# Kernel optimization log

Measured on AMD Instinct MI355X. Metric: run time of the kernel, lower is better.

The kernel has to match this reference:

```python
import jax, jax.numpy as jnp
import numpy as np

CHEB_K = 2  # hops per support; stacked terms = 1 + 2*CHEB_K = 5


def setup_inputs() -> dict:
    key = jax.random.key(0)
    k1, k2, k3, k4, k5 = jax.random.split(key, 5)
    B, N, C, O, D = 16, 1024, 64, 64, 10
    return {
        "x": jax.random.normal(k1, (B, N, C), dtype=jnp.float32),
        "adj": jax.random.uniform(k2, (2, B, N, N), dtype=jnp.float32),
        "node_embedding": jax.random.normal(k3, (N, D), dtype=jnp.float32),
        "weights_pool": jax.random.normal(k4, (D, 2 * CHEB_K + 1, C, O), dtype=jnp.float32) * 0.1,
        "bias_pool": jax.random.normal(k5, (D, O), dtype=jnp.float32) * 0.1,
    }


def reference(x, adj, node_embedding, weights_pool, bias_pool):
    # k-hop graph aggregation over each of the 2 supports
    out = [x]
    for s in range(adj.shape[0]):
        a = adj[s]  # [B, N, N]
        x1 = x
        for _ in range(CHEB_K):
            x1 = jnp.einsum('bnm,bmc->bnc', a, x1)
            out.append(x1)
    x_g = jnp.stack(out, axis=2)  # [B, N, K, C] with K = 2*cheb_k+1 (already node-major)
    # per-node hypernetwork weights and bias from node embeddings
    weights = jnp.einsum('nd,dkio->nkio', node_embedding, weights_pool)  # [N, K, C, O]
    bias = node_embedding @ bias_pool  # [N, O]
    # per-node contraction over (K, C)
    return jnp.einsum('bnki,nkio->bno', x_g, weights) + bias
```

## Files before the change

### kernel.cpp

```cpp
#include <hip/hip_runtime.h>
#include <stdint.h>


typedef __attribute__((ext_vector_type(4))) float f32x4;
typedef __attribute__((ext_vector_type(2))) float f32x2;
typedef __attribute__((ext_vector_type(8))) short s16x8;
typedef __attribute__((ext_vector_type(8))) __bf16 bf16x8;

__device__ __forceinline__ unsigned short f2bf(float f) {
  union { float f; uint32_t u; } v; v.f = f;
  uint32_t r = v.u + 0x7FFFu + ((v.u >> 16) & 1u);
  return (unsigned short)(r >> 16);
}
__device__ __forceinline__ uint32_t pack2(float a, float b) {
  return (uint32_t)f2bf(a) | ((uint32_t)f2bf(b) << 16);
}

union FragU { s16x8 s; bf16x8 b; uint32_t u[4]; };

__device__ __forceinline__ void async_cp16(const void* g, void* l) {
  __builtin_amdgcn_global_load_lds(
      (const __attribute__((address_space(1))) void*)g,
      (__attribute__((address_space(3))) void*)l, 16, 0, 0);
}

__global__ __launch_bounds__(256) void cvtprep(
    const float* __restrict__ adj, unsigned short* __restrict__ adjb,
    const float* __restrict__ x, const float* __restrict__ wp,
    unsigned short* __restrict__ XT0, unsigned short* __restrict__ X0b,
    unsigned short* __restrict__ wpTb) {
  __shared__ __align__(16) char smem[17160];
  const int tid = threadIdx.x;
  const int bid = blockIdx.x;

  if (bid < 8192) {
    const size_t stride = (size_t)8192 * 256 * 8;
    for (size_t p = ((size_t)bid * 256 + tid) * 8; p < 33554432u;
         p += stride) {
      f32x4 a = *(const f32x4*)(adj + p);
      f32x4 b = *(const f32x4*)(adj + p + 4);
      union { s16x8 s; uint32_t u[4]; } o;
      o.u[0] = pack2(a[0], a[1]);
      o.u[1] = pack2(a[2], a[3]);
      o.u[2] = pack2(b[0], b[1]);
      o.u[3] = pack2(b[2], b[3]);
      *(s16x8*)(adjb + p) = o.s;
    }
    return;
  }

  const int pid = bid - 8192;
  if (pid < 256) {
    unsigned short (*tl)[72] = (unsigned short(*)[72])smem;
    const int b = pid >> 4, n0 = (pid & 15) * 64;
    {
      const int c4 = (tid & 15) * 4;
#pragma unroll
      for (int i = 0; i < 4; ++i) {
        const int row = (tid >> 4) + i * 16;
        f32x4 v =
            *(const f32x4*)(x + ((size_t)(b * 1024 + n0 + row)) * 64 + c4);
        const uint32_t w0 = pack2(v[0], v[1]);
        const uint32_t w1 = pack2(v[2], v[3]);
        *(uint32_t*)&tl[row][c4]     = w0;
        *(uint32_t*)&tl[row][c4 + 2] = w1;
        const uint64_t wq = (uint64_t)w0 | ((uint64_t)w1 << 32);
        *(uint64_t*)(X0b + ((size_t)(b * 1024 + n0 + row)) * 64 + c4) = wq;
      }
    }
    __syncthreads();
    {
      const int c = tid >> 2;
      const int nch = (tid & 3) * 16;
      s16x8 s0, s1;
#pragma unroll
      for (int j = 0; j < 8; ++j) {
        s0[j] = (short)tl[nch + j][c];
        s1[j] = (short)tl[nch + 8 + j][c];
      }
      unsigned short* p = XT0 + (size_t)(b * 64 + c) * 1024 + n0 + nch;
      *(s16x8*)p = s0;
      *(s16x8*)(p + 8) = s1;
    }
  } else {
    float (*tl)[65] = (float(*)[65])smem;
    const int jj = pid - 256;
    const int d = jj / 5, ki0 = (jj % 5) * 64;
    const float* src = wp + (size_t)d * 20480;
    {
      const int o4 = (tid & 15) * 4;
#pragma unroll
      for (int i = 0; i < 4; ++i) {
        const int row = (tid >> 4) + i * 16;
        f32x4 v = *(const f32x4*)(src + (size_t)(ki0 + row) * 64 + o4);
        tl[row][o4] = v[0]; tl[row][o4 + 1] = v[1];
        tl[row][o4 + 2] = v[2]; tl[row][o4 + 3] = v[3];
      }
    }
    __syncthreads();
    {
      const int o = tid >> 2;
      const int kch = (tid & 3) * 16;
      unsigned short* dst =
          wpTb + (size_t)d * 20480 + (size_t)o * 320 + ki0 + kch;
      s16x8 s0, s1;
#pragma unroll
      for (int j = 0; j < 8; ++j) {
        s0[j] = (short)f2bf(tl[kch + j][o]);
        s1[j] = (short)f2bf(tl[kch + 8 + j][o]);
      }
      *(s16x8*)dst = s0;
      *(s16x8*)(dst + 8) = s1;
    }
  }
}

__device__ __forceinline__ void hop_body(
    char* smem, const unsigned short* __restrict__ A,
    const unsigned short* __restrict__ XT, unsigned short* __restrict__ Xoutb,
    unsigned short* __restrict__ XTout, int write_xt, int rowbase) {
  const int tid = threadIdx.x;
  const int wave = tid >> 6, lane = tid & 63;
  const int l15 = lane & 15, q = lane >> 4;

  unsigned short* const Ast = (unsigned short*)smem;
  unsigned short* const Bst = (unsigned short*)smem + 12288;

  const int sub = lane >> 3;
  const int ch = lane & 7;
  const unsigned short* asrc[2];
  const unsigned short* bsrc[2];
  int ldso[2];
#pragma unroll
  for (int i = 0; i < 2; ++i) {
    const int r = wave * 16 + i * 8 + sub;
    asrc[i] = A + (size_t)(rowbase + r) * 1024 + (ch ^ (r & 7)) * 8;
    bsrc[i] = XT + (size_t)r * 1024 + (ch ^ (r & 7)) * 8;
    ldso[i] = (wave * 16 + i * 8) * 64;
  }

  f32x4 acc[4];
#pragma unroll
  for (int t = 0; t < 4; ++t) acc[t] = (f32x4){0.f, 0.f, 0.f, 0.f};

  auto issue = [&](int s, int k0) {
#pragma unroll
    for (int i = 0; i < 2; ++i) {
      async_cp16(asrc[i] + k0, Ast + s * 4096 + ldso[i]);
      async_cp16(bsrc[i] + k0, Bst + s * 4096 + ldso[i]);
    }
  };
  const int sw = l15 & 7;
  auto compute = [&](int s) {
    const unsigned short* Ab = Ast + s * 4096 + (wave * 16 + l15) * 64;
    const unsigned short* Bb = Bst + s * 4096 + l15 * 64;
#pragma unroll
    for (int h = 0; h < 2; ++h) {
      const int cko = ((h * 4 + q) ^ sw) * 8;
      FragU af;
      af.s = *(const s16x8*)(Ab + cko);
#pragma unroll
      for (int t = 0; t < 4; ++t) {
        FragU bf;
        bf.s = *(const s16x8*)(Bb + t * 1024 + cko);
        acc[t] = __builtin_amdgcn_mfma_f32_16x16x32_bf16(af.b, bf.b, acc[t],
                                                         0, 0, 0);
      }
    }
  };

  issue(0, 0);
  issue(1, 64);
#pragma unroll 1
  for (int kt = 0; kt < 15; ++kt) {
    asm volatile("s_waitcnt vmcnt(4)" ::: "memory");
    __builtin_amdgcn_sched_barrier(0);
    __builtin_amdgcn_s_barrier();
    __builtin_amdgcn_sched_barrier(0);
    if (kt < 14) issue((kt + 2) % 3, (kt + 2) * 64);
    compute(kt % 3);
  }
  asm volatile("s_waitcnt vmcnt(0)" ::: "memory");
  __builtin_amdgcn_sched_barrier(0);
  __builtin_amdgcn_s_barrier();
  __builtin_amdgcn_sched_barrier(0);
  compute(0);

  __syncthreads();
  float (*tile)[65] = (float(*)[65])smem;
#pragma unroll
  for (int t = 0; t < 4; ++t)
#pragma unroll
    for (int rr = 0; rr < 4; ++rr)
      tile[wave * 16 + q * 4 + rr][t * 16 + l15] = acc[t][rr];
  __syncthreads();

  {
    const int row = tid >> 2;
    const int cb = (tid & 3) * 16;
    unsigned short* __restrict__ outp =
        Xoutb + (size_t)(rowbase + row) * 64 + cb;
    s16x8 s0, s1;
#pragma unroll
    for (int j = 0; j < 8; ++j) {
      s0[j] = (short)f2bf(tile[row][cb + j]);
      s1[j] = (short)f2bf(tile[row][cb + 8 + j]);
    }
    *(s16x8*)outp = s0;
    *(s16x8*)(outp + 8) = s1;
  }
  if (write_xt) {
    const int c = tid >> 2;
    const int nch = (tid & 3) * 16;
    unsigned short* __restrict__ xtp = XTout + (size_t)c * 1024 + rowbase + nch;
    s16x8 s0, s1;
#pragma unroll
    for (int j = 0; j < 8; ++j) {
      s0[j] = (short)f2bf(tile[nch + j][c]);
      s1[j] = (short)f2bf(tile[nch + 8 + j][c]);
    }
    *(s16x8*)xtp = s0;
    *(s16x8*)(xtp + 8) = s1;
  }
}

__global__ __launch_bounds__(256, 2) void hop1_kernel(
    const unsigned short* __restrict__ adjb,
    const unsigned short* __restrict__ XT0, unsigned short* __restrict__ X1b,
    unsigned short* __restrict__ XT1) {
  __shared__ __align__(16) char smem[49152];
  const int bx = blockIdx.x, slice = blockIdx.y, b = slice & 15;
  hop_body(smem, adjb + (size_t)slice * 1048576, XT0 + (size_t)b * 65536,
           X1b + (size_t)slice * 65536, XT1 + (size_t)slice * 65536, 1,
           bx * 64);
}

__global__ __launch_bounds__(256, 2) void hop2_kernel(
    const unsigned short* __restrict__ adjb,
    const unsigned short* __restrict__ XT1, unsigned short* __restrict__ X2b) {
  __shared__ __align__(16) char smem[49152];
  const int bx = 15 - (int)blockIdx.x;
  const int slice = 31 - (int)blockIdx.y;
  hop_body(smem, adjb + (size_t)slice * 1048576, XT1 + (size_t)slice * 65536,
           X2b + (size_t)slice * 65536, (unsigned short*)0, 0, bx * 64);
}

__global__ __launch_bounds__(256, 2) void final_kernel(
    const unsigned short* __restrict__ X0b,
    const unsigned short* __restrict__ X1b,
    const unsigned short* __restrict__ X2b,
    const unsigned short* __restrict__ wpTb, const float* __restrict__ emb,
    const float* __restrict__ bias_pool, float* __restrict__ out) {
  __shared__ unsigned short xg[2][16][328];
  const int tid = threadIdx.x;
  const int node_base = blockIdx.x * 2;

  for (int u = tid; u < 5120; u += 256) {
    const int nd = u / 2560;
    int rem = u - nd * 2560;
    const int bb = rem / 160;
    const int kiu = rem - bb * 160;
    const int ki = kiu * 2;
    const int k = ki >> 6;
    const int c = ki & 63;
    const int nn = node_base + nd;
    const unsigned short* base =
        k == 0 ? X0b
        : k == 1 ? X1b
        : k == 2 ? X2b
        : k == 3 ? X1b + 1048576 : X2b + 1048576;
    const uint32_t w =
        *(const uint32_t*)(base + ((size_t)bb * 1024 + nn) * 64 + c);
    *(uint32_t*)&xg[nd][bb][ki] = w;
  }
  __syncthreads();

  const int wave = tid >> 6, lane = tid & 63;
  const int nd = wave >> 1, oh = wave & 1;
  const int l15 = lane & 15, q = lane >> 4;
  const int n = node_base + nd;

  FragU af[10];
#pragma unroll
  for (int ks = 0; ks < 10; ++ks)
    af[ks].s = *(const s16x8*)&xg[nd][l15][ks * 32 + q * 8];

  f32x4 acc[2];
  acc[0] = (f32x4){0.f, 0.f, 0.f, 0.f};
  acc[1] = (f32x4){0.f, 0.f, 0.f, 0.f};

  const unsigned short* wb0 = wpTb + (size_t)(oh * 32 + l15) * 320 + q * 8;
#pragma unroll 1
  for (int d = 0; d < 10; ++d) {
    const unsigned short* wd = wb0 + (size_t)d * 20480;
    f32x4 tmp[2];
    tmp[0] = (f32x4){0.f, 0.f, 0.f, 0.f};
    tmp[1] = (f32x4){0.f, 0.f, 0.f, 0.f};
#pragma unroll
    for (int ks = 0; ks < 10; ++ks) {
#pragma unroll
      for (int tt = 0; tt < 2; ++tt) {
        FragU bf;
        bf.s = *(const s16x8*)(wd + tt * 5120 + ks * 32);
        tmp[tt] = __builtin_amdgcn_mfma_f32_16x16x32_bf16(af[ks].b, bf.b,
                                                          tmp[tt], 0, 0, 0);
      }
    }
    const float e = emb[n * 10 + d];
#pragma unroll
    for (int tt = 0; tt < 2; ++tt)
#pragma unroll
      for (int rr = 0; rr < 4; ++rr)
        acc[tt][rr] += e * tmp[tt][rr];
  }

#pragma unroll
  for (int tt = 0; tt < 2; ++tt) {
    const int o = (oh * 2 + tt) * 16 + l15;
    float bv = 0.f;
#pragma unroll
    for (int d = 0; d < 10; ++d)
      bv += emb[n * 10 + d] * bias_pool[d * 64 + o];
#pragma unroll
    for (int rr = 0; rr < 4; ++rr) {
      const int bb = q * 4 + rr;
      out[((size_t)bb * 1024 + n) * 64 + o] = acc[tt][rr] + bv;
    }
  }
}

extern "C" void kernel_launch(void* const* d_in, const int* in_sizes, int n_in,
                              void* d_out, int out_size, void* d_ws,
                              size_t ws_size, hipStream_t stream) {
  const float* x   = (const float*)d_in[0];
  const float* adj = (const float*)d_in[1];
  const float* emb = (const float*)d_in[2];
  const float* wp  = (const float*)d_in[3];
  const float* bp  = (const float*)d_in[4];
  float* out = (float*)d_out;

  char* ws = (char*)d_ws;
  unsigned short* adjb = (unsigned short*)(ws);
  unsigned short* XT0  = (unsigned short*)(ws + ((size_t)68 << 20));
  unsigned short* XT1  = (unsigned short*)(ws + ((size_t)70 << 20));
  unsigned short* X0b  = (unsigned short*)(ws + ((size_t)74 << 20));
  unsigned short* X1b  = (unsigned short*)(ws + ((size_t)76 << 20));
  unsigned short* X2b  = (unsigned short*)(ws + ((size_t)80 << 20));
  unsigned short* wpTb = (unsigned short*)(ws + ((size_t)84 << 20));

  cvtprep<<<dim3(8498), dim3(256), 0, stream>>>(adj, adjb, x, wp, XT0, X0b,
                                                wpTb);
  hop1_kernel<<<dim3(16, 32), dim3(256), 0, stream>>>(adjb, XT0, X1b, XT1);
  hop2_kernel<<<dim3(16, 32), dim3(256), 0, stream>>>(adjb, XT1, X2b);
  final_kernel<<<dim3(512), dim3(256), 0, stream>>>(X0b, X1b, X2b, wpTb, emb,
                                                    bp, out);
}
```

Measured before the change: 290.6 us.

## Split adj conversion kernel, double-buffer hop loop, stage weights in LDS for final

Splits the combined prep kernel into a separate adj bf16 conversion kernel and a small x/weight prep kernel. The hop kernels move from a 3-stage async pipeline to a 2-stage double buffer with plain syncthreads, which cuts LDS so launch bounds can target 4 blocks per CU. The final kernel uses 512 threads covering 4 nodes per block: it loads X fragments straight from global and stages each d-slice of the swizzled weight table into LDS with async copies shared across the nodes. Fewer pipeline stages may expose more load latency in the hop GEMMs, and the final kernel now waits on a full sync for every d iteration.

```diff
diff --git a/kernel.cpp b/kernel.cpp
--- a/kernel.cpp
+++ b/kernel.cpp
@@ -3,7 +3,6 @@
 
 
 typedef __attribute__((ext_vector_type(4))) float f32x4;
-typedef __attribute__((ext_vector_type(2))) float f32x2;
 typedef __attribute__((ext_vector_type(8))) short s16x8;
 typedef __attribute__((ext_vector_type(8))) __bf16 bf16x8;
 
@@ -24,35 +23,33 @@
       (__attribute__((address_space(3))) void*)l, 16, 0, 0);
 }
 
-__global__ __launch_bounds__(256) void cvtprep(
-    const float* __restrict__ adj, unsigned short* __restrict__ adjb,
-    const float* __restrict__ x, const float* __restrict__ wp,
-    unsigned short* __restrict__ XT0, unsigned short* __restrict__ X0b,
-    unsigned short* __restrict__ wpTb) {
+__global__ __launch_bounds__(256) void cvt_adj(const float* __restrict__ adj,
+                                               unsigned short* __restrict__ adjb) {
+  const size_t stride = (size_t)gridDim.x * 256 * 8;
+  for (size_t p = ((size_t)blockIdx.x * 256 + threadIdx.x) * 8;
+       p < 33554432u; p += stride) {
+    f32x4 a = *(const f32x4*)(adj + p);
+    f32x4 b = *(const f32x4*)(adj + p + 4);
+    union { s16x8 s; uint32_t u[4]; } o;
+    o.u[0] = pack2(a[0], a[1]);
+    o.u[1] = pack2(a[2], a[3]);
+    o.u[2] = pack2(b[0], b[1]);
+    o.u[3] = pack2(b[2], b[3]);
+    *(s16x8*)(adjb + p) = o.s;
+  }
+}
+
+__global__ __launch_bounds__(256) void prep(const float* __restrict__ x,
+                                            const float* __restrict__ wp,
+                                            unsigned short* __restrict__ XT0,
+                                            unsigned short* __restrict__ X0b,
+                                            unsigned short* __restrict__ wpTb) {
   __shared__ __align__(16) char smem[17160];
   const int tid = threadIdx.x;
   const int bid = blockIdx.x;
-
-  if (bid < 8192) {
-    const size_t stride = (size_t)8192 * 256 * 8;
-    for (size_t p = ((size_t)bid * 256 + tid) * 8; p < 33554432u;
-         p += stride) {
-      f32x4 a = *(const f32x4*)(adj + p);
-      f32x4 b = *(const f32x4*)(adj + p + 4);
-      union { s16x8 s; uint32_t u[4]; } o;
-      o.u[0] = pack2(a[0], a[1]);
-      o.u[1] = pack2(a[2], a[3]);
-      o.u[2] = pack2(b[0], b[1]);
-      o.u[3] = pack2(b[2], b[3]);
-      *(s16x8*)(adjb + p) = o.s;
-    }
-    return;
-  }
-
-  const int pid = bid - 8192;
-  if (pid < 256) {
+  if (bid < 256) {
     unsigned short (*tl)[72] = (unsigned short(*)[72])smem;
-    const int b = pid >> 4, n0 = (pid & 15) * 64;
+    const int b = bid >> 4, n0 = (bid & 15) * 64;
     {
       const int c4 = (tid & 15) * 4;
 #pragma unroll
@@ -84,7 +81,7 @@
     }
   } else {
     float (*tl)[65] = (float(*)[65])smem;
-    const int jj = pid - 256;
+    const int jj = bid - 256;
     const int d = jj / 5, ki0 = (jj % 5) * 64;
     const float* src = wp + (size_t)d * 20480;
     {
@@ -101,16 +98,16 @@
     {
       const int o = tid >> 2;
       const int kch = (tid & 3) * 16;
-      unsigned short* dst =
-          wpTb + (size_t)d * 20480 + (size_t)o * 320 + ki0 + kch;
       s16x8 s0, s1;
 #pragma unroll
       for (int j = 0; j < 8; ++j) {
         s0[j] = (short)f2bf(tl[kch + j][o]);
         s1[j] = (short)f2bf(tl[kch + 8 + j][o]);
       }
-      *(s16x8*)dst = s0;
-      *(s16x8*)(dst + 8) = s1;
+      const int c0 = (ki0 + kch) >> 3;
+      unsigned short* base = wpTb + (size_t)d * 24576 + (size_t)o * 384;
+      *(s16x8*)(base + ((c0) ^ (o & 7)) * 8) = s0;
+      *(s16x8*)(base + ((c0 + 1) ^ (o & 7)) * 8) = s1;
     }
   }
 }
@@ -124,7 +121,7 @@
   const int l15 = lane & 15, q = lane >> 4;
 
   unsigned short* const Ast = (unsigned short*)smem;
-  unsigned short* const Bst = (unsigned short*)smem + 12288;
+  unsigned short* const Bst = (unsigned short*)smem + 8192;
 
   const int sub = lane >> 3;
   const int ch = lane & 7;
@@ -170,21 +167,13 @@
   };
 
   issue(0, 0);
-  issue(1, 64);
 #pragma unroll 1
-  for (int kt = 0; kt < 15; ++kt) {
-    asm volatile("s_waitcnt vmcnt(4)" ::: "memory");
-    __builtin_amdgcn_sched_barrier(0);
-    __builtin_amdgcn_s_barrier();
-    __builtin_amdgcn_sched_barrier(0);
-    if (kt < 14) issue((kt + 2) % 3, (kt + 2) * 64);
-    compute(kt % 3);
-  }
-  asm volatile("s_waitcnt vmcnt(0)" ::: "memory");
-  __builtin_amdgcn_sched_barrier(0);
-  __builtin_amdgcn_s_barrier();
-  __builtin_amdgcn_sched_barrier(0);
-  compute(0);
+  for (int kt = 0; kt < 16; ++kt) {
+    const int cur = kt & 1;
+    __syncthreads();
+    if (kt + 1 < 16) issue(cur ^ 1, (kt + 1) * 64);
+    compute(cur);
+  }
 
   __syncthreads();
   float (*tile)[65] = (float(*)[65])smem;
@@ -224,107 +213,100 @@
   }
 }
 
-__global__ __launch_bounds__(256, 2) void hop1_kernel(
+__global__ __launch_bounds__(256, 4) void hop1_kernel(
     const unsigned short* __restrict__ adjb,
     const unsigned short* __restrict__ XT0, unsigned short* __restrict__ X1b,
     unsigned short* __restrict__ XT1) {
-  __shared__ __align__(16) char smem[49152];
+  __shared__ __align__(16) char smem[32768];
   const int bx = blockIdx.x, slice = blockIdx.y, b = slice & 15;
   hop_body(smem, adjb + (size_t)slice * 1048576, XT0 + (size_t)b * 65536,
            X1b + (size_t)slice * 65536, XT1 + (size_t)slice * 65536, 1,
            bx * 64);
 }
 
-__global__ __launch_bounds__(256, 2) void hop2_kernel(
+__global__ __launch_bounds__(256, 4) void hop2_kernel(
     const unsigned short* __restrict__ adjb,
     const unsigned short* __restrict__ XT1, unsigned short* __restrict__ X2b) {
-  __shared__ __align__(16) char smem[49152];
+  __shared__ __align__(16) char smem[32768];
   const int bx = 15 - (int)blockIdx.x;
   const int slice = 31 - (int)blockIdx.y;
   hop_body(smem, adjb + (size_t)slice * 1048576, XT1 + (size_t)slice * 65536,
            X2b + (size_t)slice * 65536, (unsigned short*)0, 0, bx * 64);
 }
 
-__global__ __launch_bounds__(256, 2) void final_kernel(
+__global__ __launch_bounds__(512, 4) void final_kernel(
     const unsigned short* __restrict__ X0b,
     const unsigned short* __restrict__ X1b,
     const unsigned short* __restrict__ X2b,
     const unsigned short* __restrict__ wpTb, const float* __restrict__ emb,
-    const float* __restrict__ bias_pool, float* __restrict__ out) {
-  __shared__ unsigned short xg[2][16][328];
-  const int tid = threadIdx.x;
-  const int node_base = blockIdx.x * 2;
-
-  for (int u = tid; u < 5120; u += 256) {
-    const int nd = u / 2560;
-    int rem = u - nd * 2560;
-    const int bb = rem / 160;
-    const int kiu = rem - bb * 160;
-    const int ki = kiu * 2;
-    const int k = ki >> 6;
-    const int c = ki & 63;
-    const int nn = node_base + nd;
-    const unsigned short* base =
-        k == 0 ? X0b
-        : k == 1 ? X1b
-        : k == 2 ? X2b
-        : k == 3 ? X1b + 1048576 : X2b + 1048576;
-    const uint32_t w =
-        *(const uint32_t*)(base + ((size_t)bb * 1024 + nn) * 64 + c);
-    *(uint32_t*)&xg[nd][bb][ki] = w;
-  }
-  __syncthreads();
-
+    const float* __restrict__ bp, float* __restrict__ out) {
+  __shared__ __align__(16) unsigned short wd[64][384];
+  const int tid = threadIdx.x, bid = blockIdx.x;
   const int wave = tid >> 6, lane = tid & 63;
+  const int l15 = lane & 15, q = lane >> 4;
   const int nd = wave >> 1, oh = wave & 1;
-  const int l15 = lane & 15, q = lane >> 4;
-  const int n = node_base + nd;
-
-  FragU af[10];
-#pragma unroll
-  for (int ks = 0; ks < 10; ++ks)
-    af[ks].s = *(const s16x8*)&xg[nd][l15][ks * 32 + q * 8];
-
-  f32x4 acc[2];
-  acc[0] = (f32x4){0.f, 0.f, 0.f, 0.f};
-  acc[1] = (f32x4){0.f, 0.f, 0.f, 0.f};
-
-  const unsigned short* wb0 = wpTb + (size_t)(oh * 32 + l15) * 320 + q * 8;
+  const int n = bid * 4 + nd;
+  const int sw2 = l15 & 7;
+
+  FragU af10[10];
+#pragma unroll
+  for (int ks = 0; ks < 10; ++ks) {
+    const int k = ks >> 1;
+    const int cc0 = (ks & 1) * 32 + q * 8;
+    const unsigned short* srcp;
+    if (k == 0) {
+      srcp = X0b + ((size_t)l15 * 1024 + n) * 64 + cc0;
+    } else {
+      const unsigned short* arr = (k == 1 || k == 3) ? X1b : X2b;
+      const int s = (k >= 3) ? 1 : 0;
+      srcp = arr + ((size_t)(s * 16 + l15) * 1024 + n) * 64 + cc0;
+    }
+    af10[ks].s = *(const s16x8*)srcp;
+  }
+
+  f32x4 acc0 = {0.f, 0.f, 0.f, 0.f}, acc1 = {0.f, 0.f, 0.f, 0.f};
+  const unsigned short* wsrc = wpTb + (size_t)wave * 3072 + lane * 8;
+  unsigned short* wdst = (unsigned short*)wd + wave * 3072;
 #pragma unroll 1
   for (int d = 0; d < 10; ++d) {
-    const unsigned short* wd = wb0 + (size_t)d * 20480;
-    f32x4 tmp[2];
-    tmp[0] = (f32x4){0.f, 0.f, 0.f, 0.f};
-    tmp[1] = (f32x4){0.f, 0.f, 0.f, 0.f};
+    if (d) __syncthreads();
+#pragma unroll
+    for (int i = 0; i < 6; ++i)
+      async_cp16(wsrc + (size_t)d * 24576 + i * 512, wdst + i * 512);
+    asm volatile("s_waitcnt vmcnt(0)" ::: "memory");
+    __builtin_amdgcn_sched_barrier(0);
+    __syncthreads();
+    f32x4 t0 = {0.f, 0.f, 0.f, 0.f}, t1 = {0.f, 0.f, 0.f, 0.f};
 #pragma unroll
     for (int ks = 0; ks < 10; ++ks) {
-#pragma unroll
-      for (int tt = 0; tt < 2; ++tt) {
-        FragU bf;
-        bf.s = *(const s16x8*)(wd + tt * 5120 + ks * 32);
-        tmp[tt] = __builtin_amdgcn_mfma_f32_16x16x32_bf16(af[ks].b, bf.b,
-                                                          tmp[tt], 0, 0, 0);
-      }
+      const int p = ((ks * 4 + q) ^ sw2) * 8;
+      FragU b0, b1;
+      b0.s = *(const s16x8*)&wd[oh * 32 + l15][p];
+      b1.s = *(const s16x8*)&wd[oh * 32 + 16 + l15][p];
+      t0 = __builtin_amdgcn_mfma_f32_16x16x32_bf16(af10[ks].b, b0.b, t0,
+                                                   0, 0, 0);
+      t1 = __builtin_amdgcn_mfma_f32_16x16x32_bf16(af10[ks].b, b1.b, t1,
+                                                   0, 0, 0);
     }
     const float e = emb[n * 10 + d];
 #pragma unroll
-    for (int tt = 0; tt < 2; ++tt)
-#pragma unroll
-      for (int rr = 0; rr < 4; ++rr)
-        acc[tt][rr] += e * tmp[tt][rr];
+    for (int rr = 0; rr < 4; ++rr) {
+      acc0[rr] += e * t0[rr];
+      acc1[rr] += e * t1[rr];
+    }
   }
 
 #pragma unroll
   for (int tt = 0; tt < 2; ++tt) {
-    const int o = (oh * 2 + tt) * 16 + l15;
+    const int o = oh * 32 + tt * 16 + l15;
     float bv = 0.f;
 #pragma unroll
-    for (int d = 0; d < 10; ++d)
-      bv += emb[n * 10 + d] * bias_pool[d * 64 + o];
+    for (int d = 0; d < 10; ++d) bv += emb[n * 10 + d] * bp[d * 64 + o];
 #pragma unroll
     for (int rr = 0; rr < 4; ++rr) {
       const int bb = q * 4 + rr;
-      out[((size_t)bb * 1024 + n) * 64 + o] = acc[tt][rr] + bv;
+      const float a = tt ? acc1[rr] : acc0[rr];
+      out[((size_t)bb * 1024 + n) * 64 + o] = a + bv;
     }
   }
 }
@@ -348,10 +330,10 @@
   unsigned short* X2b  = (unsigned short*)(ws + ((size_t)80 << 20));
   unsigned short* wpTb = (unsigned short*)(ws + ((size_t)84 << 20));
 
-  cvtprep<<<dim3(8498), dim3(256), 0, stream>>>(adj, adjb, x, wp, XT0, X0b,
-                                                wpTb);
+  cvt_adj<<<dim3(8192), dim3(256), 0, stream>>>(adj, adjb);
+  prep<<<dim3(306), dim3(256), 0, stream>>>(x, wp, XT0, X0b, wpTb);
   hop1_kernel<<<dim3(16, 32), dim3(256), 0, stream>>>(adjb, XT0, X1b, XT1);
   hop2_kernel<<<dim3(16, 32), dim3(256), 0, stream>>>(adjb, XT1, X2b);
-  final_kernel<<<dim3(512), dim3(256), 0, stream>>>(X0b, X1b, X2b, wpTb, emb,
+  final_kernel<<<dim3(256), dim3(512), 0, stream>>>(X0b, X1b, X2b, wpTb, emb,
                                                     bp, out);
 }
```

New measurement: 259.7 us. 1.12x faster.
